# Optimization experiments

Hardware: AMD Instinct MI355X
Metric: run time of the kernel (lower is better)

## Reference

```python
import jax, jax.numpy as jnp
import numpy as np

H, D_MODEL = 12, 768
D_K = D_MODEL // H
B, S = 2, 2048


def setup_inputs() -> dict:
    key = jax.random.key(0)
    ks = jax.random.split(key, 11)
    sc = 0.02
    return {
        "query": jax.random.normal(ks[0], (B, S, D_MODEL), jnp.float32),
        "key": jax.random.normal(ks[1], (B, S, D_MODEL), jnp.float32),
        "value": jax.random.normal(ks[2], (B, S, D_MODEL), jnp.float32),
        # per-head Linear weights, torch layout [out, in] -> stacked [h, d_k, d_model]
        "Wq": jax.random.normal(ks[3], (H, D_K, D_MODEL), jnp.float32) * sc,
        "bq": jax.random.normal(ks[4], (H, D_K), jnp.float32) * sc,
        "Wk": jax.random.normal(ks[5], (H, D_K, D_MODEL), jnp.float32) * sc,
        "bk": jax.random.normal(ks[6], (H, D_K), jnp.float32) * sc,
        "Wv": jax.random.normal(ks[7], (H, D_K, D_MODEL), jnp.float32) * sc,
        "bv": jax.random.normal(ks[8], (H, D_K), jnp.float32) * sc,
        "Wo": jax.random.normal(ks[9], (D_MODEL, D_MODEL), jnp.float32) * sc,
        "bo": jax.random.normal(ks[10], (D_MODEL,), jnp.float32) * sc,
    }


def reference(query, key, value, Wq, bq, Wk, bk, Wv, bv, Wo, bo):
    # per-head projections: [B,S,D] x [H,Dk,D] -> [B,H,S,Dk]
    q = jnp.einsum("bsd,hkd->bhsk", query, Wq) + bq[None, :, None, :]
    k = jnp.einsum("bsd,hkd->bhsk", key, Wk) + bk[None, :, None, :]
    v = jnp.einsum("bsd,hkd->bhsk", value, Wv) + bv[None, :, None, :]
    # scaled dot-product attention (full [B,H,S,S] scores, as in the original)
    scores = jnp.einsum("bhqk,bhsk->bhqs", q, k) * (1.0 / jnp.sqrt(jnp.asarray(D_K, q.dtype)))
    attn = jax.nn.softmax(scores, axis=-1)
    ctx = jnp.einsum("bhqs,bhsk->bhqk", attn, v)
    # merge heads: [B,H,S,Dk] -> [B,S,H*Dk]
    ctx = ctx.transpose(0, 2, 1, 3).reshape(query.shape[0], -1, H * D_K)
    # output projection (torch Linear: x @ W.T + b)
    return ctx @ Wo.T + bo
```

## Files before the change

### kernel.cpp

```cpp
#include <hip/hip_runtime.h>
#include <math.h>
#include <stdint.h>

#define H_  12
#define DK_ 64
#define DM_ 768
#define B_  2
#define S_  2048

typedef __bf16 bf16x8 __attribute__((ext_vector_type(8)));
typedef __bf16 bf16x4_t __attribute__((ext_vector_type(4)));
typedef float  f32x4  __attribute__((ext_vector_type(4)));

__device__ __forceinline__ void gload16(const void* gsrc, void* ldst) {
    using GPtr = const __attribute__((address_space(1))) void*;
    using LPtr = __attribute__((address_space(3))) void*;
    __builtin_amdgcn_global_load_lds((GPtr)(uintptr_t)gsrc, (LPtr)(uintptr_t)ldst, 16, 0, 0);
}

__device__ __forceinline__ void bar() {
    asm volatile("" ::: "memory");
    __builtin_amdgcn_s_barrier();
    asm volatile("" ::: "memory");
}
__device__ __forceinline__ void bar_end() {
    asm volatile("s_waitcnt lgkmcnt(0)" ::: "memory");
    __builtin_amdgcn_s_barrier();
    asm volatile("" ::: "memory");
}
#define WAITVM(N) asm volatile("s_waitcnt vmcnt(" #N ")" ::: "memory")

template<int OFF>
__device__ __forceinline__ bf16x8 trread8(uint32_t addr) {
    union { bf16x8 v; bf16x4_t h[2]; } u;
    asm volatile("ds_read_b64_tr_b16 %0, %2 offset:%3\n\t"
                 "ds_read_b64_tr_b16 %1, %2 offset:%4"
                 : "=v"(u.h[0]), "=v"(u.h[1])
                 : "v"(addr), "i"(OFF), "i"(OFF + 128));
    return u.v;
}

__global__ __launch_bounds__(256)
void prep(const float* __restrict__ q, const float* __restrict__ k,
          const float* __restrict__ v,
          const float* __restrict__ wq, const float* __restrict__ wk,
          const float* __restrict__ wv, const float* __restrict__ wo,
          __bf16* __restrict__ qo, __bf16* __restrict__ ko, __bf16* __restrict__ vo,
          __bf16* __restrict__ wqh, __bf16* __restrict__ wkh,
          __bf16* __restrict__ wvh, __bf16* __restrict__ woh,
          __bf16* __restrict__ wol)
{
    const int NIN = 786432;
    int gid = blockIdx.x * 256 + threadIdx.x;
    if (gid < 3 * NIN) {
        int which = gid / NIN, i = gid - which * NIN;
        const float* src = which == 0 ? q : (which == 1 ? k : v);
        __bf16* dst = which == 0 ? qo : (which == 1 ? ko : vo);
        float4 a = ((const float4*)src)[i];
        bf16x4_t h;
        h[0]=(__bf16)a.x; h[1]=(__bf16)a.y; h[2]=(__bf16)a.z; h[3]=(__bf16)a.w;
        *(bf16x4_t*)&dst[i*4] = h;
    } else {
        int i = gid - 3 * NIN;
        float4 a; bf16x4_t h, l;
        a = ((const float4*)wq)[i];
        h[0]=(__bf16)a.x; h[1]=(__bf16)a.y; h[2]=(__bf16)a.z; h[3]=(__bf16)a.w;
        *(bf16x4_t*)&wqh[i*4] = h;
        a = ((const float4*)wk)[i];
        h[0]=(__bf16)a.x; h[1]=(__bf16)a.y; h[2]=(__bf16)a.z; h[3]=(__bf16)a.w;
        *(bf16x4_t*)&wkh[i*4] = h;
        a = ((const float4*)wv)[i];
        h[0]=(__bf16)a.x; h[1]=(__bf16)a.y; h[2]=(__bf16)a.z; h[3]=(__bf16)a.w;
        *(bf16x4_t*)&wvh[i*4] = h;
        a = ((const float4*)wo)[i];
        h[0]=(__bf16)a.x; h[1]=(__bf16)a.y; h[2]=(__bf16)a.z; h[3]=(__bf16)a.w;
        l[0]=(__bf16)(a.x-(float)h[0]); l[1]=(__bf16)(a.y-(float)h[1]);
        l[2]=(__bf16)(a.z-(float)h[2]); l[3]=(__bf16)(a.w-(float)h[3]);
        *(bf16x4_t*)&woh[i*4] = h;
        *(bf16x4_t*)&wol[i*4] = l;
    }
}

__global__ __launch_bounds__(256)
void proj_gemm(const __bf16* __restrict__ x0, const __bf16* __restrict__ x1,
               const __bf16* __restrict__ x2,
               const __bf16* __restrict__ w0, const __bf16* __restrict__ w1,
               const __bf16* __restrict__ w2,
               const float* __restrict__ b0, const float* __restrict__ b1,
               const float* __restrict__ b2,
               __bf16* __restrict__ o0, __bf16* __restrict__ o1,
               __bf16* __restrict__ o2,
               float s0, float s1, float s2)
{
    __shared__ __align__(16) __bf16 sA[2][64 * 64];
    __shared__ __align__(16) __bf16 sW[2][128 * 64];

    const int tid = threadIdx.x;
    const int w = tid >> 6, lane = tid & 63;
    const int g = lane >> 4, c16 = lane & 15;
    const int wr = w >> 1, wc = w & 1;

    const int z = blockIdx.z;
    const __bf16* A  = z == 0 ? x0 : (z == 1 ? x1 : x2);
    const __bf16* W  = z == 0 ? w0 : (z == 1 ? w1 : w2);
    const float* bias = z == 0 ? b0 : (z == 1 ? b1 : b2);
    __bf16* out = z == 0 ? o0 : (z == 1 ? o1 : o2);
    const float scale = z == 0 ? s0 : (z == 1 ? s1 : s2);

    int flat = blockIdx.y * 6 + blockIdx.x;
    int swz  = (flat & 7) * 48 + (flat >> 3);
    int nx = swz % 6, my = swz / 6;
    const int m0 = my * 64, n0 = nx * 128;

    const int rj  = tid >> 3;
    const int rsw = ((tid & 7) ^ (rj & 7)) << 3;
    const __bf16* asrc = A + (size_t)(m0 + rj) * 768 + rsw;
    const __bf16* wsrc = W + (size_t)(n0 + rj) * 768 + rsw;

    f32x4 acc[2][4] = {};

    auto STAGE = [&](int kk, int buf) {
        #pragma unroll
        for (int i = 0; i < 2; ++i)
            gload16(asrc + (size_t)(i * 32) * 768 + kk,
                    (char*)&sA[buf][0] + (i * 256 + tid) * 16);
        #pragma unroll
        for (int i = 0; i < 4; ++i)
            gload16(wsrc + (size_t)(i * 32) * 768 + kk,
                    (char*)&sW[buf][0] + (i * 256 + tid) * 16);
    };

    STAGE(0, 0);
    int cur = 0;
    for (int k0 = 0; k0 < 768; k0 += 64) {
        if (k0 + 64 < 768) { STAGE(k0 + 64, cur ^ 1); WAITVM(6); }
        else               { WAITVM(0); }
        bar();
        const __bf16* Ab = &sA[cur][0];
        const __bf16* Wb = &sW[cur][0];
        #pragma unroll
        for (int ks = 0; ks < 2; ++ks) {
            bf16x8 ah[2];
            #pragma unroll
            for (int rt = 0; rt < 2; ++rt) {
                int j = wr * 32 + rt * 16 + c16;
                ah[rt] = *(const bf16x8*)&Ab[j * 64 + ((((ks << 2) | g) ^ (j & 7)) << 3)];
            }
            __builtin_amdgcn_s_setprio(1);
            #pragma unroll
            for (int ct = 0; ct < 4; ++ct) {
                int j = wc * 64 + ct * 16 + c16;
                bf16x8 bh = *(const bf16x8*)&Wb[j * 64 + ((((ks << 2) | g) ^ (j & 7)) << 3)];
                #pragma unroll
                for (int rt = 0; rt < 2; ++rt)
                    acc[rt][ct] = __builtin_amdgcn_mfma_f32_16x16x32_bf16(ah[rt], bh, acc[rt][ct], 0, 0, 0);
            }
            __builtin_amdgcn_s_setprio(0);
        }
        bar_end();
        cur ^= 1;
    }

    #pragma unroll
    for (int rt = 0; rt < 2; ++rt)
        #pragma unroll
        for (int ct = 0; ct < 4; ++ct) {
            int n = n0 + wc * 64 + ct * 16 + c16;
            float bv = bias[n];
            #pragma unroll
            for (int e = 0; e < 4; ++e) {
                int m = m0 + wr * 32 + rt * 16 + g * 4 + e;
                float val = (acc[rt][ct][e] + bv) * scale;
                int b = m >> 11, s = m & (S_ - 1);
                int h = n >> 6,  dk = n & 63;
                out[(((size_t)b * H_ + h) * S_ + s) * DK_ + dk] = (__bf16)val;
            }
        }
}

__global__ __launch_bounds__(256)
void out_gemm(const __bf16* __restrict__ Ah, const __bf16* __restrict__ Al,
              const __bf16* __restrict__ Wh, const __bf16* __restrict__ Wl,
              const float* __restrict__ bias, float* __restrict__ out)
{
    __shared__ __align__(16) __bf16 sAh[2][64*64], sAl[2][64*64];
    __shared__ __align__(16) __bf16 sWh[2][64*64], sWl[2][64*64];

    const int tid = threadIdx.x;
    const int w = tid >> 6, lane = tid & 63;
    const int g = lane >> 4, c16 = lane & 15;
    const int wr = w >> 1, wc = w & 1;

    int flat = blockIdx.y * 12 + blockIdx.x;
    int swz  = (flat & 7) * 96 + (flat >> 3);
    int nx = swz % 12, my = swz / 12;
    const int m0 = my * 64, n0 = nx * 64;

    const int rj  = tid >> 3;
    const int rsw = ((tid & 7) ^ (rj & 7)) << 3;
    const __bf16* ahs = Ah + (size_t)(m0 + rj) * 768 + rsw;
    const __bf16* als = Al + (size_t)(m0 + rj) * 768 + rsw;
    const __bf16* whs = Wh + (size_t)(n0 + rj) * 768 + rsw;
    const __bf16* wls = Wl + (size_t)(n0 + rj) * 768 + rsw;

    f32x4 acc[2][2] = {};

    auto STAGE = [&](int kk, int buf) {
        #pragma unroll
        for (int i = 0; i < 2; ++i) {
            size_t so = (size_t)(i * 32) * 768 + kk;
            int dof = (i * 256 + tid) * 16;
            gload16(ahs + so, (char*)&sAh[buf][0] + dof);
            gload16(als + so, (char*)&sAl[buf][0] + dof);
            gload16(whs + so, (char*)&sWh[buf][0] + dof);
            gload16(wls + so, (char*)&sWl[buf][0] + dof);
        }
    };

    STAGE(0, 0);
    int cur = 0;
    for (int k0 = 0; k0 < 768; k0 += 64) {
        if (k0 + 64 < 768) { STAGE(k0 + 64, cur ^ 1); WAITVM(8); }
        else               { WAITVM(0); }
        bar();
        #pragma unroll
        for (int ks = 0; ks < 2; ++ks) {
            bf16x8 va[2], la[2];
            #pragma unroll
            for (int rt = 0; rt < 2; ++rt) {
                int j = wr * 32 + rt * 16 + c16;
                int off = j * 64 + ((((ks << 2) | g) ^ (j & 7)) << 3);
                va[rt] = *(const bf16x8*)&sAh[cur][off];
                la[rt] = *(const bf16x8*)&sAl[cur][off];
            }
            __builtin_amdgcn_s_setprio(1);
            #pragma unroll
            for (int ct = 0; ct < 2; ++ct) {
                int j = wc * 32 + ct * 16 + c16;
                int off = j * 64 + ((((ks << 2) | g) ^ (j & 7)) << 3);
                bf16x8 bh = *(const bf16x8*)&sWh[cur][off];
                bf16x8 bl = *(const bf16x8*)&sWl[cur][off];
                #pragma unroll
                for (int rt = 0; rt < 2; ++rt) {
                    acc[rt][ct] = __builtin_amdgcn_mfma_f32_16x16x32_bf16(va[rt], bh, acc[rt][ct], 0, 0, 0);
                    acc[rt][ct] = __builtin_amdgcn_mfma_f32_16x16x32_bf16(la[rt], bh, acc[rt][ct], 0, 0, 0);
                    acc[rt][ct] = __builtin_amdgcn_mfma_f32_16x16x32_bf16(va[rt], bl, acc[rt][ct], 0, 0, 0);
                }
            }
            __builtin_amdgcn_s_setprio(0);
        }
        bar_end();
        cur ^= 1;
    }

    #pragma unroll
    for (int rt = 0; rt < 2; ++rt)
        #pragma unroll
        for (int ct = 0; ct < 2; ++ct) {
            int n = n0 + wc * 32 + ct * 16 + c16;
            float bv = bias[n];
            #pragma unroll
            for (int e = 0; e < 4; ++e) {
                int m = m0 + wr * 32 + rt * 16 + g * 4 + e;
                out[(size_t)m * 768 + n] = acc[rt][ct][e] + bv;
            }
        }
}

__global__ __launch_bounds__(256)
void attn_mfma(const __bf16* __restrict__ q, const __bf16* __restrict__ k,
               const __bf16* __restrict__ v,
               __bf16* __restrict__ ch, __bf16* __restrict__ cl)
{
    __shared__ __align__(16) __bf16 Ksm[2][64 * 64];
    __shared__ __align__(16) __bf16 Vsm[2][64 * 64];
    __shared__ __align__(16) __bf16 Psm[4][16 * 64];

    const int tid  = threadIdx.x;
    const int w    = tid >> 6;
    const int lane = tid & 63;
    const int g    = lane >> 4;
    const int c16  = lane & 15;

    int swzb = (blockIdx.x & 7) * 96 + (blockIdx.x >> 3);
    const int bh = swzb >> 5;
    const int q0 = (swzb & 31) * 64 + w * 16;
    const size_t base = (size_t)bh * S_ * DK_;

    bf16x8 qa[2];
    {
        const __bf16* qrow = q + base + (size_t)(q0 + c16) * DK_ + g * 8;
        qa[0] = *(const bf16x8*)(qrow);
        qa[1] = *(const bf16x8*)(qrow + 32);
    }

    f32x4 oacc[4] = {};
    float lr = 0.f;
    char* Pw = (char*)&Psm[w][0];
    const int psw = (c16 & 7);

    const int kj   = tid >> 3;
    const int ksw  = ((tid & 7) ^ (kj & 7)) << 3;
    const __bf16* ksrc0 = k + base + (size_t)kj * 64 + ksw;
    const int vkey = (tid >> 1) & 63;
    const int vt0  = tid >> 7;
    const int vhf  = (tid & 1) << 3;
    const __bf16* vsrc0 = v + base + (size_t)vkey * 64 + vhf;

    auto STAGE = [&](int kb, int buf) {
        #pragma unroll
        for (int i = 0; i < 2; ++i)
            gload16(ksrc0 + (size_t)(kb + i * 32) * 64,
                    (char*)&Ksm[buf][0] + (i * 256 + tid) * 16);
        #pragma unroll
        for (int i = 0; i < 2; ++i)
            gload16(vsrc0 + (size_t)kb * 64 + (vt0 + 2 * i) * 16,
                    (char*)&Vsm[buf][0] + (i * 256 + tid) * 16);
    };

    STAGE(0, 0);
    int cur = 0;
    for (int kb = 0; kb < S_; kb += 64) {
        if (kb + 64 < S_) { STAGE(kb + 64, cur ^ 1); WAITVM(4); }
        else              { WAITVM(0); }
        bar();

        const __bf16* Kb = &Ksm[cur][0];
        f32x4 sacc[4];
        #pragma unroll
        for (int t = 0; t < 4; ++t) {
            int krow = t * 16 + c16;
            f32x4 s_ = {};
            #pragma unroll
            for (int s = 0; s < 2; ++s) {
                bf16x8 kf = *(const bf16x8*)&Kb[krow * 64 + ((((s << 2) | g) ^ (krow & 7)) << 3)];
                s_ = __builtin_amdgcn_mfma_f32_16x16x32_bf16(kf, qa[s], s_, 0, 0, 0);
            }
            sacc[t] = s_;
        }

        float csum = 0.f;
        #pragma unroll
        for (int t = 0; t < 4; ++t) {
            float p0 = exp2f(sacc[t][0]);
            float p1 = exp2f(sacc[t][1]);
            float p2 = exp2f(sacc[t][2]);
            float p3 = exp2f(sacc[t][3]);
            csum += (p0 + p1) + (p2 + p3);
            bf16x4_t pk;
            pk[0] = (__bf16)p0; pk[1] = (__bf16)p1;
            pk[2] = (__bf16)p2; pk[3] = (__bf16)p3;
            int c = 2 * t + (g >> 1);
            *(bf16x4_t*)(Pw + c16 * 128 + ((c ^ psw) << 4) + (g & 1) * 8) = pk;
        }
        lr += csum;

        uint32_t va = (uint32_t)(uintptr_t)&Vsm[cur][g * 128 + 4 * c16];
        {
            bf16x8 pa = *(const bf16x8*)(Pw + c16 * 128 + ((g ^ psw) << 4));
            bf16x8 v0 = trread8<0>(va);
            bf16x8 v1 = trread8<2048>(va);
            bf16x8 v2 = trread8<4096>(va);
            bf16x8 v3 = trread8<6144>(va);
            asm volatile("s_waitcnt lgkmcnt(0)" ::: "memory");
            __builtin_amdgcn_sched_barrier(0);
            __builtin_amdgcn_s_setprio(1);
            oacc[0] = __builtin_amdgcn_mfma_f32_16x16x32_bf16(pa, v0, oacc[0], 0, 0, 0);
            oacc[1] = __builtin_amdgcn_mfma_f32_16x16x32_bf16(pa, v1, oacc[1], 0, 0, 0);
            oacc[2] = __builtin_amdgcn_mfma_f32_16x16x32_bf16(pa, v2, oacc[2], 0, 0, 0);
            oacc[3] = __builtin_amdgcn_mfma_f32_16x16x32_bf16(pa, v3, oacc[3], 0, 0, 0);
            __builtin_amdgcn_s_setprio(0);
        }
        {
            bf16x8 pa = *(const bf16x8*)(Pw + c16 * 128 + (((4 | g) ^ psw) << 4));
            bf16x8 v0 = trread8<1024>(va);
            bf16x8 v1 = trread8<3072>(va);
            bf16x8 v2 = trread8<5120>(va);
            bf16x8 v3 = trread8<7168>(va);
            asm volatile("s_waitcnt lgkmcnt(0)" ::: "memory");
            __builtin_amdgcn_sched_barrier(0);
            __builtin_amdgcn_s_setprio(1);
            oacc[0] = __builtin_amdgcn_mfma_f32_16x16x32_bf16(pa, v0, oacc[0], 0, 0, 0);
            oacc[1] = __builtin_amdgcn_mfma_f32_16x16x32_bf16(pa, v1, oacc[1], 0, 0, 0);
            oacc[2] = __builtin_amdgcn_mfma_f32_16x16x32_bf16(pa, v2, oacc[2], 0, 0, 0);
            oacc[3] = __builtin_amdgcn_mfma_f32_16x16x32_bf16(pa, v3, oacc[3], 0, 0, 0);
            __builtin_amdgcn_s_setprio(0);
        }
        bar_end();
        cur ^= 1;
    }

    lr += __shfl_xor(lr, 16, 64);
    lr += __shfl_xor(lr, 32, 64);

    int b = bh / H_, h = bh % H_;
    #pragma unroll
    for (int r = 0; r < 4; ++r) {
        int srcl = (lane & 48) | (g * 4 + r);
        float lsum = __shfl(lr, srcl, 64);
        float inv = 1.0f / lsum;
        int row = q0 + g * 4 + r;
        size_t o = ((size_t)b * S_ + row) * DM_ + h * DK_ + c16;
        #pragma unroll
        for (int t = 0; t < 4; ++t) {
            float val = oacc[t][r] * inv;
            __bf16 hi = (__bf16)val;
            ch[o + t * 16] = hi;
            cl[o + t * 16] = (__bf16)(val - (float)hi);
        }
    }
}

extern "C" void kernel_launch(void* const* d_in, const int* in_sizes, int n_in,
                              void* d_out, int out_size, void* d_ws, size_t ws_size,
                              hipStream_t stream)
{
    const float* query = (const float*)d_in[0];
    const float* key   = (const float*)d_in[1];
    const float* value = (const float*)d_in[2];
    const float* Wq    = (const float*)d_in[3];
    const float* bq    = (const float*)d_in[4];
    const float* Wk    = (const float*)d_in[5];
    const float* bk    = (const float*)d_in[6];
    const float* Wv    = (const float*)d_in[7];
    const float* bv    = (const float*)d_in[8];
    const float* Wo    = (const float*)d_in[9];
    const float* bo    = (const float*)d_in[10];
    float* out = (float*)d_out;

    const size_t TSZ = (size_t)B_ * S_ * DM_;
    const size_t WSZ = (size_t)DM_ * DM_;
    __bf16* p  = (__bf16*)d_ws;
    __bf16* xq = p;
    __bf16* xk = xq + TSZ;
    __bf16* xv = xk + TSZ;
    __bf16* qh = xv + TSZ;
    __bf16* kh = qh + TSZ;
    __bf16* vh = kh + TSZ;
    __bf16* wqh = vh + TSZ;
    __bf16* wkh = wqh + WSZ;
    __bf16* wvh = wkh + WSZ;
    __bf16* woh = wvh + WSZ;
    __bf16* wol = woh + WSZ;
    __bf16* chh = xq;
    __bf16* cll = xk;

    prep<<<9792, 256, 0, stream>>>(query, key, value, Wq, Wk, Wv, Wo,
                                   xq, xk, xv, wqh, wkh, wvh, woh, wol);

    dim3 gp(6, 64, 3);
    proj_gemm<<<gp, 256, 0, stream>>>(xq, xk, xv, wqh, wkh, wvh,
                                      bq, bk, bv, qh, kh, vh,
                                      0.18033688011112f, 1.0f, 1.0f);

    attn_mfma<<<768, 256, 0, stream>>>(qh, kh, vh, chh, cll);

    dim3 go(12, 64);
    out_gemm<<<go, 256, 0, stream>>>(chh, cll, woh, wol, bo, out);
}
```

Before: 106.7 us.

## Process two 16-row query tiles per wave with 128-thread attention blocks

The attention kernel now runs 2 waves per block instead of 4, and each wave handles 32 query rows as two 16-row tiles. Each K fragment and V transposed read from LDS is reused across two sets of MFMAs. This halves LDS traffic per query row and gives each wave more independent MFMA work. In exchange each wave uses more registers for its two accumulator sets, each thread issues more staging loads, and fewer waves per block are available to hide latency.

Measured after the change: 116.3 us. +9.1%, slower.

```diff
diff --git a/kernel.cpp b/kernel.cpp
--- a/kernel.cpp
+++ b/kernel.cpp
@@ -267,14 +267,14 @@
         }
 }
 
-__global__ __launch_bounds__(256)
+__global__ __launch_bounds__(128)
 void attn_mfma(const __bf16* __restrict__ q, const __bf16* __restrict__ k,
                const __bf16* __restrict__ v,
                __bf16* __restrict__ ch, __bf16* __restrict__ cl)
 {
     __shared__ __align__(16) __bf16 Ksm[2][64 * 64];
     __shared__ __align__(16) __bf16 Vsm[2][64 * 64];
-    __shared__ __align__(16) __bf16 Psm[4][16 * 64];
+    __shared__ __align__(16) __bf16 Psm[2][32 * 64];
 
     const int tid  = threadIdx.x;
     const int w    = tid >> 6;
@@ -283,81 +283,91 @@
     const int c16  = lane & 15;
 
     int swzb = (blockIdx.x & 7) * 96 + (blockIdx.x >> 3);
-    const int bh = swzb >> 5;
-    const int q0 = (swzb & 31) * 64 + w * 16;
+    const int bh    = swzb >> 5;
+    const int qbase = (swzb & 31) * 64 + w * 32;
     const size_t base = (size_t)bh * S_ * DK_;
 
-    bf16x8 qa[2];
-    {
-        const __bf16* qrow = q + base + (size_t)(q0 + c16) * DK_ + g * 8;
-        qa[0] = *(const bf16x8*)(qrow);
-        qa[1] = *(const bf16x8*)(qrow + 32);
-    }
-
-    f32x4 oacc[4] = {};
-    float lr = 0.f;
+    bf16x8 qa[2][2];
+    #pragma unroll
+    for (int qt = 0; qt < 2; ++qt) {
+        const __bf16* qrow = q + base + (size_t)(qbase + qt * 16 + c16) * DK_ + g * 8;
+        qa[qt][0] = *(const bf16x8*)(qrow);
+        qa[qt][1] = *(const bf16x8*)(qrow + 32);
+    }
+
+    f32x4 oacc0[4] = {}, oacc1[4] = {};
+    float lr0 = 0.f, lr1 = 0.f;
     char* Pw = (char*)&Psm[w][0];
     const int psw = (c16 & 7);
 
     const int kj   = tid >> 3;
     const int ksw  = ((tid & 7) ^ (kj & 7)) << 3;
     const __bf16* ksrc0 = k + base + (size_t)kj * 64 + ksw;
-    const int vkey = (tid >> 1) & 63;
-    const int vt0  = tid >> 7;
+    const int vkey = tid >> 1;
     const int vhf  = (tid & 1) << 3;
     const __bf16* vsrc0 = v + base + (size_t)vkey * 64 + vhf;
 
     auto STAGE = [&](int kb, int buf) {
         #pragma unroll
-        for (int i = 0; i < 2; ++i)
-            gload16(ksrc0 + (size_t)(kb + i * 32) * 64,
-                    (char*)&Ksm[buf][0] + (i * 256 + tid) * 16);
-        #pragma unroll
-        for (int i = 0; i < 2; ++i)
-            gload16(vsrc0 + (size_t)kb * 64 + (vt0 + 2 * i) * 16,
-                    (char*)&Vsm[buf][0] + (i * 256 + tid) * 16);
+        for (int i = 0; i < 4; ++i)
+            gload16(ksrc0 + (size_t)(kb + i * 16) * 64,
+                    (char*)&Ksm[buf][0] + (i * 128 + tid) * 16);
+        #pragma unroll
+        for (int i = 0; i < 4; ++i)
+            gload16(vsrc0 + (size_t)kb * 64 + i * 16,
+                    (char*)&Vsm[buf][0] + (i * 128 + tid) * 16);
     };
 
     STAGE(0, 0);
     int cur = 0;
     for (int kb = 0; kb < S_; kb += 64) {
-        if (kb + 64 < S_) { STAGE(kb + 64, cur ^ 1); WAITVM(4); }
+        if (kb + 64 < S_) { STAGE(kb + 64, cur ^ 1); WAITVM(8); }
         else              { WAITVM(0); }
         bar();
 
         const __bf16* Kb = &Ksm[cur][0];
-        f32x4 sacc[4];
+        f32x4 sacc0[4] = {}, sacc1[4] = {};
         #pragma unroll
         for (int t = 0; t < 4; ++t) {
             int krow = t * 16 + c16;
-            f32x4 s_ = {};
             #pragma unroll
             for (int s = 0; s < 2; ++s) {
                 bf16x8 kf = *(const bf16x8*)&Kb[krow * 64 + ((((s << 2) | g) ^ (krow & 7)) << 3)];
-                s_ = __builtin_amdgcn_mfma_f32_16x16x32_bf16(kf, qa[s], s_, 0, 0, 0);
-            }
-            sacc[t] = s_;
-        }
-
-        float csum = 0.f;
+                sacc0[t] = __builtin_amdgcn_mfma_f32_16x16x32_bf16(kf, qa[0][s], sacc0[t], 0, 0, 0);
+                sacc1[t] = __builtin_amdgcn_mfma_f32_16x16x32_bf16(kf, qa[1][s], sacc1[t], 0, 0, 0);
+            }
+        }
+
+        float cs0 = 0.f, cs1 = 0.f;
         #pragma unroll
         for (int t = 0; t < 4; ++t) {
-            float p0 = exp2f(sacc[t][0]);
-            float p1 = exp2f(sacc[t][1]);
-            float p2 = exp2f(sacc[t][2]);
-            float p3 = exp2f(sacc[t][3]);
-            csum += (p0 + p1) + (p2 + p3);
-            bf16x4_t pk;
-            pk[0] = (__bf16)p0; pk[1] = (__bf16)p1;
-            pk[2] = (__bf16)p2; pk[3] = (__bf16)p3;
             int c = 2 * t + (g >> 1);
-            *(bf16x4_t*)(Pw + c16 * 128 + ((c ^ psw) << 4) + (g & 1) * 8) = pk;
-        }
-        lr += csum;
+            int coff = ((c ^ psw) << 4) + (g & 1) * 8;
+            {
+                float p0 = exp2f(sacc0[t][0]), p1 = exp2f(sacc0[t][1]);
+                float p2 = exp2f(sacc0[t][2]), p3 = exp2f(sacc0[t][3]);
+                cs0 += (p0 + p1) + (p2 + p3);
+                bf16x4_t pk;
+                pk[0] = (__bf16)p0; pk[1] = (__bf16)p1;
+                pk[2] = (__bf16)p2; pk[3] = (__bf16)p3;
+                *(bf16x4_t*)(Pw + c16 * 128 + coff) = pk;
+            }
+            {
+                float p0 = exp2f(sacc1[t][0]), p1 = exp2f(sacc1[t][1]);
+                float p2 = exp2f(sacc1[t][2]), p3 = exp2f(sacc1[t][3]);
+                cs1 += (p0 + p1) + (p2 + p3);
+                bf16x4_t pk;
+                pk[0] = (__bf16)p0; pk[1] = (__bf16)p1;
+                pk[2] = (__bf16)p2; pk[3] = (__bf16)p3;
+                *(bf16x4_t*)(Pw + 2048 + c16 * 128 + coff) = pk;
+            }
+        }
+        lr0 += cs0; lr1 += cs1;
 
         uint32_t va = (uint32_t)(uintptr_t)&Vsm[cur][g * 128 + 4 * c16];
         {
-            bf16x8 pa = *(const bf16x8*)(Pw + c16 * 128 + ((g ^ psw) << 4));
+            bf16x8 pa0 = *(const bf16x8*)(Pw + c16 * 128 + ((g ^ psw) << 4));
+            bf16x8 pa1 = *(const bf16x8*)(Pw + 2048 + c16 * 128 + ((g ^ psw) << 4));
             bf16x8 v0 = trread8<0>(va);
             bf16x8 v1 = trread8<2048>(va);
             bf16x8 v2 = trread8<4096>(va);
@@ -365,14 +375,19 @@
             asm volatile("s_waitcnt lgkmcnt(0)" ::: "memory");
             __builtin_amdgcn_sched_barrier(0);
             __builtin_amdgcn_s_setprio(1);
-            oacc[0] = __builtin_amdgcn_mfma_f32_16x16x32_bf16(pa, v0, oacc[0], 0, 0, 0);
-            oacc[1] = __builtin_amdgcn_mfma_f32_16x16x32_bf16(pa, v1, oacc[1], 0, 0, 0);
-            oacc[2] = __builtin_amdgcn_mfma_f32_16x16x32_bf16(pa, v2, oacc[2], 0, 0, 0);
-            oacc[3] = __builtin_amdgcn_mfma_f32_16x16x32_bf16(pa, v3, oacc[3], 0, 0, 0);
+            oacc0[0] = __builtin_amdgcn_mfma_f32_16x16x32_bf16(pa0, v0, oacc0[0], 0, 0, 0);
+            oacc1[0] = __builtin_amdgcn_mfma_f32_16x16x32_bf16(pa1, v0, oacc1[0], 0, 0, 0);
+            oacc0[1] = __builtin_amdgcn_mfma_f32_16x16x32_bf16(pa0, v1, oacc0[1], 0, 0, 0);
+            oacc1[1] = __builtin_amdgcn_mfma_f32_16x16x32_bf16(pa1, v1, oacc1[1], 0, 0, 0);
+            oacc0[2] = __builtin_amdgcn_mfma_f32_16x16x32_bf16(pa0, v2, oacc0[2], 0, 0, 0);
+            oacc1[2] = __builtin_amdgcn_mfma_f32_16x16x32_bf16(pa1, v2, oacc1[2], 0, 0, 0);
+            oacc0[3] = __builtin_amdgcn_mfma_f32_16x16x32_bf16(pa0, v3, oacc0[3], 0, 0, 0);
+            oacc1[3] = __builtin_amdgcn_mfma_f32_16x16x32_bf16(pa1, v3, oacc1[3], 0, 0, 0);
             __builtin_amdgcn_s_setprio(0);
         }
         {
-            bf16x8 pa = *(const bf16x8*)(Pw + c16 * 128 + (((4 | g) ^ psw) << 4));
+            bf16x8 pa0 = *(const bf16x8*)(Pw + c16 * 128 + (((4 | g) ^ psw) << 4));
+            bf16x8 pa1 = *(const bf16x8*)(Pw + 2048 + c16 * 128 + (((4 | g) ^ psw) << 4));
             bf16x8 v0 = trread8<1024>(va);
             bf16x8 v1 = trread8<3072>(va);
             bf16x8 v2 = trread8<5120>(va);
@@ -380,33 +395,44 @@
             asm volatile("s_waitcnt lgkmcnt(0)" ::: "memory");
             __builtin_amdgcn_sched_barrier(0);
             __builtin_amdgcn_s_setprio(1);
-            oacc[0] = __builtin_amdgcn_mfma_f32_16x16x32_bf16(pa, v0, oacc[0], 0, 0, 0);
-            oacc[1] = __builtin_amdgcn_mfma_f32_16x16x32_bf16(pa, v1, oacc[1], 0, 0, 0);
-            oacc[2] = __builtin_amdgcn_mfma_f32_16x16x32_bf16(pa, v2, oacc[2], 0, 0, 0);
-            oacc[3] = __builtin_amdgcn_mfma_f32_16x16x32_bf16(pa, v3, oacc[3], 0, 0, 0);
+            oacc0[0] = __builtin_amdgcn_mfma_f32_16x16x32_bf16(pa0, v0, oacc0[0], 0, 0, 0);
+            oacc1[0] = __builtin_amdgcn_mfma_f32_16x16x32_bf16(pa1, v0, oacc1[0], 0, 0, 0);
+            oacc0[1] = __builtin_amdgcn_mfma_f32_16x16x32_bf16(pa0, v1, oacc0[1], 0, 0, 0);
+            oacc1[1] = __builtin_amdgcn_mfma_f32_16x16x32_bf16(pa1, v1, oacc1[1], 0, 0, 0);
+            oacc0[2] = __builtin_amdgcn_mfma_f32_16x16x32_bf16(pa0, v2, oacc0[2], 0, 0, 0);
+            oacc1[2] = __builtin_amdgcn_mfma_f32_16x16x32_bf16(pa1, v2, oacc1[2], 0, 0, 0);
+            oacc0[3] = __builtin_amdgcn_mfma_f32_16x16x32_bf16(pa0, v3, oacc0[3], 0, 0, 0);
+            oacc1[3] = __builtin_amdgcn_mfma_f32_16x16x32_bf16(pa1, v3, oacc1[3], 0, 0, 0);
             __builtin_amdgcn_s_setprio(0);
         }
         bar_end();
         cur ^= 1;
     }
 
-    lr += __shfl_xor(lr, 16, 64);
-    lr += __shfl_xor(lr, 32, 64);
+    lr0 += __shfl_xor(lr0, 16, 64);
+    lr0 += __shfl_xor(lr0, 32, 64);
+    lr1 += __shfl_xor(lr1, 16, 64);
+    lr1 += __shfl_xor(lr1, 32, 64);
 
     int b = bh / H_, h = bh % H_;
     #pragma unroll
-    for (int r = 0; r < 4; ++r) {
-        int srcl = (lane & 48) | (g * 4 + r);
-        float lsum = __shfl(lr, srcl, 64);
-        float inv = 1.0f / lsum;
-        int row = q0 + g * 4 + r;
-        size_t o = ((size_t)b * S_ + row) * DM_ + h * DK_ + c16;
-        #pragma unroll
-        for (int t = 0; t < 4; ++t) {
-            float val = oacc[t][r] * inv;
-            __bf16 hi = (__bf16)val;
-            ch[o + t * 16] = hi;
-            cl[o + t * 16] = (__bf16)(val - (float)hi);
+    for (int qt = 0; qt < 2; ++qt) {
+        const f32x4* oa = qt == 0 ? oacc0 : oacc1;
+        float lrq = qt == 0 ? lr0 : lr1;
+        #pragma unroll
+        for (int r = 0; r < 4; ++r) {
+            int srcl = (lane & 48) | (g * 4 + r);
+            float lsum = __shfl(lrq, srcl, 64);
+            float inv = 1.0f / lsum;
+            int row = qbase + qt * 16 + g * 4 + r;
+            size_t o = ((size_t)b * S_ + row) * DM_ + h * DK_ + c16;
+            #pragma unroll
+            for (int t = 0; t < 4; ++t) {
+                float val = oa[t][r] * inv;
+                __bf16 hi = (__bf16)val;
+                ch[o + t * 16] = hi;
+                cl[o + t * 16] = (__bf16)(val - (float)hi);
+            }
         }
     }
 }
@@ -453,7 +479,7 @@
                                       bq, bk, bv, qh, kh, vh,
                                       0.18033688011112f, 1.0f, 1.0f);
 
-    attn_mfma<<<768, 256, 0, stream>>>(qh, kh, vh, chh, cll);
+    attn_mfma<<<768, 128, 0, stream>>>(qh, kh, vh, chh, cll);
 
     dim3 go(12, 64);
     out_gemm<<<go, 256, 0, stream>>>(chh, cll, woh, wol, bo, out);
```
